# Performance work log

Hardware: AMD Instinct MI355X
Metric: run time of the kernel (lower is better)

The kernel has to match this reference:

```python
import jax, jax.numpy as jnp
import numpy as np

C = 512
IC = C // 2
BN_EPS = 1e-5

def conv1x1(x, w, b):
    # x: (b,c,h,w), w: (o,c), b: (o,)
    return jnp.einsum('bchw,oc->bohw', x, w) + b[None, :, None, None]

def setup_inputs() -> dict:
    key = jax.random.key(0)
    ks = jax.random.split(key, 9)
    b, h, w = 8, 48, 48
    x = jax.random.normal(ks[0], (b, C, h, w), dtype=jnp.float32)
    s = 1.0 / np.sqrt(C)
    g_w = jax.random.normal(ks[1], (IC, C), dtype=jnp.float32) * s
    g_b = jnp.zeros((IC,), jnp.float32)
    theta_w = jax.random.normal(ks[2], (IC, C), dtype=jnp.float32) * s
    theta_b = jnp.zeros((IC,), jnp.float32)
    phi_w = jax.random.normal(ks[3], (IC, C), dtype=jnp.float32) * s
    phi_b = jnp.zeros((IC,), jnp.float32)
    w_w = jax.random.normal(ks[4], (C, IC), dtype=jnp.float32) * (1.0 / np.sqrt(IC))
    w_b = jnp.zeros((C,), jnp.float32)
    # BatchNorm affine params: initialized to 0 per nn.init.constant_ in source
    bn_gamma = jnp.zeros((C,), jnp.float32)
    bn_beta = jnp.zeros((C,), jnp.float32)
    return {"x": x, "g_w": g_w, "g_b": g_b, "theta_w": theta_w, "theta_b": theta_b,
            "phi_w": phi_w, "phi_b": phi_b, "w_w": w_w, "w_b": w_b,
            "bn_gamma": bn_gamma, "bn_beta": bn_beta}

def reference(x, g_w, g_b, theta_w, theta_b, phi_w, phi_b, w_w, w_b, bn_gamma, bn_beta):
    b, c, h, w = x.shape
    hw = h * w
    g_x = conv1x1(x, g_w, g_b).reshape(b, IC, hw).transpose(0, 2, 1)      # (b,hw,ic)
    theta_x = conv1x1(x, theta_w, theta_b).reshape(b, IC, hw).transpose(0, 2, 1)  # (b,hw,ic)
    phi_x = conv1x1(x, phi_w, phi_b).reshape(b, IC, hw)                    # (b,ic,hw)
    f = jnp.einsum('bqc,bck->bqk', theta_x, phi_x)                         # (b,hw,hw), unscaled
    f_div_C = jax.nn.softmax(f, axis=-1)
    y = jnp.einsum('bqk,bkc->bqc', f_div_C, g_x)                           # (b,hw,ic)
    y = y.transpose(0, 2, 1).reshape(b, IC, h, w)
    wy = conv1x1(y, w_w, w_b)                                              # (b,c,h,w)
    # BatchNorm2d in training mode: batch statistics over (b,h,w)
    mean = jnp.mean(wy, axis=(0, 2, 3), keepdims=True)
    var = jnp.var(wy, axis=(0, 2, 3), keepdims=True)
    wy_bn = (wy - mean) / jnp.sqrt(var + BN_EPS)
    wy_bn = wy_bn * bn_gamma[None, :, None, None] + bn_beta[None, :, None, None]
    return wy_bn + x
```

## Files before the change

kernel.cpp:

```cpp
#include <hip/hip_runtime.h>
#include <hip/hip_bf16.h>
#include <stdint.h>

constexpr int Bn  = 8;
constexpr int Cc  = 512;
constexpr int ICc = 256;
constexpr int HWc = 48 * 48;
constexpr float BN_EPS = 1e-5f;

typedef unsigned short u16;
typedef __attribute__((ext_vector_type(8))) short short8;
typedef __attribute__((ext_vector_type(4))) float f32x4;

__device__ __forceinline__ u16 f2bf(float f) {
    uint32_t u = __builtin_bit_cast(uint32_t, f);
    u += 0x7fffu + ((u >> 16) & 1u);
    return (u16)(u >> 16);
}
__device__ __forceinline__ float bf2f(u16 h) {
    uint32_t u = ((uint32_t)h) << 16;
    return __builtin_bit_cast(float, u);
}
__device__ __forceinline__ void load_lds16(const void* g, void* l) {
    __builtin_amdgcn_global_load_lds(
        (const __attribute__((address_space(1))) void*)(uintptr_t)g,
        (__attribute__((address_space(3))) void*)(uintptr_t)l, 16, 0, 0);
}

__global__ __launch_bounds__(256)
void cast_front(const float* __restrict__ th_w, const float* __restrict__ ph_w,
                const float* __restrict__ g_w, const float* __restrict__ th_b,
                const float* __restrict__ ph_b, u16* __restrict__ wcat,
                float* __restrict__ bias_thph) {
    int idx = blockIdx.x * 256 + threadIdx.x;
    if (idx < 98304) {
        const float4* src;
        if (idx < 32768)       src = (const float4*)th_w + idx;
        else if (idx < 65536)  src = (const float4*)ph_w + (idx - 32768);
        else                   src = (const float4*)g_w  + (idx - 65536);
        float4 v = *src;
        ushort4 o;
        o.x = f2bf(v.x); o.y = f2bf(v.y); o.z = f2bf(v.z); o.w = f2bf(v.w);
        ((ushort4*)wcat)[idx] = o;
    } else if (idx < 98816) {
        int i = idx - 98304;
        bias_thph[i] = (i < 256) ? th_b[i] : ph_b[i - 256];
    }
}

__global__ __launch_bounds__(256)
void cast_w(const float* __restrict__ a, u16* __restrict__ out) {
    int idx = blockIdx.x * 256 + threadIdx.x;
    float4 v = ((const float4*)a)[idx];
    ushort4 o;
    o.x = f2bf(v.x); o.y = f2bf(v.y); o.z = f2bf(v.z); o.w = f2bf(v.w);
    ((ushort4*)out)[idx] = o;
}

__global__ __launch_bounds__(256)
void transpose_cast_x(const float* __restrict__ x, u16* __restrict__ xt) {
    __shared__ float t[64][33];
    const int b = blockIdx.z;
    const int p0 = blockIdx.x * 32;
    const int c0 = blockIdx.y * 64;
    const int tx = threadIdx.x & 31, ty = threadIdx.x >> 5;
    const float* xb = x + (size_t)b * Cc * HWc;
#pragma unroll
    for (int r = 0; r < 8; ++r)
        t[r * 8 + ty][tx] = xb[(size_t)(c0 + r * 8 + ty) * HWc + p0 + tx];
    __syncthreads();
    u16* xtb = xt + (size_t)b * HWc * Cc;
    const int cc = (threadIdx.x & 31) * 2, pp = threadIdx.x >> 5;
#pragma unroll
    for (int r = 0; r < 4; ++r) {
        int p = r * 8 + pp;
        ushort2 v;
        v.x = f2bf(t[cc][p]);
        v.y = f2bf(t[cc + 1][p]);
        *(ushort2*)&xtb[(size_t)(p0 + p) * Cc + c0 + cc] = v;
    }
}

template <int TM, int STORE, bool STATS>
__global__ __launch_bounds__(256, 2)
void mfma_gemm(const u16* __restrict__ A, const u16* __restrict__ B,
               void* __restrict__ Cout, const float* __restrict__ bias,
               int bias_mode, int K, int ldA, int ldB, int ldC,
               size_t sA, size_t sB, size_t sC,
               float* __restrict__ s0g, float* __restrict__ s1g) {
    constexpr int MI = TM / 32;
    __shared__ __align__(16) u16 As[TM * 32];
    __shared__ __align__(16) u16 Bs[128 * 32];
    const int bz = blockIdx.z;
    const int m0 = blockIdx.y * TM, n0 = blockIdx.x * 128;
    const u16* Ab = A + (size_t)bz * sA + (size_t)m0 * ldA;
    const u16* Bb = B + (size_t)bz * sB + (size_t)n0 * ldB;
    const int tid = threadIdx.x, lane = tid & 63, w = tid >> 6;
    const int wm = (w & 1) * (TM / 2);
    const int wn = (w >> 1) * 64;
    const int quad = lane >> 4, m16 = lane & 15;

    f32x4 acc[MI][4];
#pragma unroll
    for (int i = 0; i < MI; ++i)
#pragma unroll
        for (int j = 0; j < 4; ++j) acc[i][j] = (f32x4){0.f, 0.f, 0.f, 0.f};

    const int L0 = 2 * w * 64 + lane, L1 = L0 + 64;
    const int br0 = L0 >> 2, bc0 = (L0 & 3) * 8;
    const int br1 = L1 >> 2, bc1 = (L1 & 3) * 8;
    const int ar0 = (TM == 128) ? br0 : (tid >> 2);
    const int ac0 = (TM == 128) ? bc0 : (tid & 3) * 8;

    for (int k0 = 0; k0 < K; k0 += 32) {
        if (TM == 128) {
            load_lds16(Ab + (size_t)ar0 * ldA + k0 + ac0, &As[2 * w * 512]);
            load_lds16(Ab + (size_t)br1 * ldA + k0 + bc1, &As[(2 * w + 1) * 512]);
        } else {
            load_lds16(Ab + (size_t)ar0 * ldA + k0 + ac0, &As[w * 512]);
        }
        load_lds16(Bb + (size_t)br0 * ldB + k0 + bc0, &Bs[2 * w * 512]);
        load_lds16(Bb + (size_t)br1 * ldB + k0 + bc1, &Bs[(2 * w + 1) * 512]);
        __syncthreads();

        short8 af[MI], bfv[4];
#pragma unroll
        for (int i = 0; i < MI; ++i)
            af[i] = *(const short8*)&As[(wm + i * 16 + m16) * 32 + quad * 8];
#pragma unroll
        for (int j = 0; j < 4; ++j)
            bfv[j] = *(const short8*)&Bs[(wn + j * 16 + m16) * 32 + quad * 8];
#pragma unroll
        for (int i = 0; i < MI; ++i)
#pragma unroll
            for (int j = 0; j < 4; ++j)
                acc[i][j] = __builtin_amdgcn_mfma_f32_16x16x32_bf16(
                    af[i], bfv[j], acc[i][j], 0, 0, 0);
        __syncthreads();
    }

    if (bias_mode) {
#pragma unroll
        for (int i = 0; i < MI; ++i)
#pragma unroll
            for (int j = 0; j < 4; ++j)
#pragma unroll
                for (int r = 0; r < 4; ++r)
                    acc[i][j][r] += (bias_mode == 2)
                        ? bias[m0 + wm + i * 16 + quad * 4 + r]
                        : bias[n0 + wn + j * 16 + m16];
    }

    if (STORE == 0) {
        u16* C = (u16*)Cout + (size_t)bz * sC;
#pragma unroll
        for (int i = 0; i < MI; ++i) {
            int m = m0 + wm + i * 16 + quad * 4;
#pragma unroll
            for (int j = 0; j < 4; ++j) {
                int n = n0 + wn + j * 16 + m16;
#pragma unroll
                for (int r = 0; r < 4; ++r)
                    C[(size_t)(m + r) * ldC + n] = f2bf(acc[i][j][r]);
            }
        }
    } else {
        float* C = (float*)Cout + (size_t)bz * sC;
#pragma unroll
        for (int i = 0; i < MI; ++i) {
            int m = m0 + wm + i * 16 + quad * 4;
#pragma unroll
            for (int j = 0; j < 4; ++j) {
                int n = n0 + wn + j * 16 + m16;
#pragma unroll
                for (int r = 0; r < 4; ++r)
                    C[(size_t)(m + r) * ldC + n] = acc[i][j][r];
            }
        }
    }

    if (STATS) {
#pragma unroll
        for (int i = 0; i < MI; ++i) {
#pragma unroll
            for (int r = 0; r < 4; ++r) {
                float v0 = 0.f, v1 = 0.f;
#pragma unroll
                for (int j = 0; j < 4; ++j) {
                    float v = acc[i][j][r];
                    v0 += v;
                    v1 = fmaf(v, v, v1);
                }
#pragma unroll
                for (int off = 8; off; off >>= 1) {
                    v0 += __shfl_down(v0, off, 16);
                    v1 += __shfl_down(v1, off, 16);
                }
                if (m16 == 0) {
                    int m = m0 + wm + i * 16 + quad * 4 + r;
                    atomicAdd(&s0g[m], v0);
                    atomicAdd(&s1g[m], v1);
                }
            }
        }
    }
}

__global__ __launch_bounds__(192)
void softmax_rows(u16* __restrict__ S) {
    const int b = blockIdx.x & 7;
    const int q = blockIdx.x >> 3;
    u16* row = S + ((size_t)b * HWc + q) * (size_t)HWc;
    const int tid = threadIdx.x;

    float v[12];
#pragma unroll
    for (int c = 0; c < 3; ++c) {
        uint2 raw = *(const uint2*)&row[(c * 192 + tid) * 4];
        v[c * 4 + 0] = bf2f((u16)(raw.x & 0xffff));
        v[c * 4 + 1] = bf2f((u16)(raw.x >> 16));
        v[c * 4 + 2] = bf2f((u16)(raw.y & 0xffff));
        v[c * 4 + 3] = bf2f((u16)(raw.y >> 16));
    }
    float m = v[0];
#pragma unroll
    for (int i = 1; i < 12; ++i) m = fmaxf(m, v[i]);
#pragma unroll
    for (int off = 32; off; off >>= 1) m = fmaxf(m, __shfl_down(m, off, 64));
    __shared__ float redm[3], reds[3];
    if ((tid & 63) == 0) redm[tid >> 6] = m;
    __syncthreads();
    m = fmaxf(fmaxf(redm[0], redm[1]), redm[2]);

    float s = 0.f;
#pragma unroll
    for (int i = 0; i < 12; ++i) { v[i] = __expf(v[i] - m); s += v[i]; }
#pragma unroll
    for (int off = 32; off; off >>= 1) s += __shfl_down(s, off, 64);
    if ((tid & 63) == 0) reds[tid >> 6] = s;
    __syncthreads();
    const float rinv = 1.0f / (reds[0] + reds[1] + reds[2]);

#pragma unroll
    for (int c = 0; c < 3; ++c) {
        uint2 o;
        o.x = (uint32_t)f2bf(v[c * 4 + 0] * rinv) |
              ((uint32_t)f2bf(v[c * 4 + 1] * rinv) << 16);
        o.y = (uint32_t)f2bf(v[c * 4 + 2] * rinv) |
              ((uint32_t)f2bf(v[c * 4 + 3] * rinv) << 16);
        *(uint2*)&row[(c * 192 + tid) * 4] = o;
    }
}

__global__ __launch_bounds__(256)
void bn_apply(const float* __restrict__ wy, const float* __restrict__ x,
              const float* __restrict__ s0, const float* __restrict__ s1,
              const float* __restrict__ gamma, const float* __restrict__ beta,
              float* __restrict__ out) {
    const size_t i4 = (size_t)blockIdx.x * 256 + threadIdx.x;
    const size_t base = i4 * 4;
    const int o = (int)((base / HWc) % Cc);
    const float N = (float)(Bn * HWc);
    const float mean = s0[o] / N;
    const float var  = s1[o] / N - mean * mean;
    const float rstd = rsqrtf(var + BN_EPS);
    const float ga = gamma[o];
    const float be = beta[o];
    const float4 w4 = ((const float4*)wy)[i4];
    const float4 x4 = ((const float4*)x)[i4];
    float4 r;
    r.x = (w4.x - mean) * rstd * ga + be + x4.x;
    r.y = (w4.y - mean) * rstd * ga + be + x4.y;
    r.z = (w4.z - mean) * rstd * ga + be + x4.z;
    r.w = (w4.w - mean) * rstd * ga + be + x4.w;
    ((float4*)out)[i4] = r;
}

extern "C" void kernel_launch(void* const* d_in, const int* in_sizes, int n_in,
                              void* d_out, int out_size, void* d_ws, size_t ws_size,
                              hipStream_t stream) {
    const float* x     = (const float*)d_in[0];
    const float* g_w   = (const float*)d_in[1];
    const float* g_b   = (const float*)d_in[2];
    const float* th_w  = (const float*)d_in[3];
    const float* th_b  = (const float*)d_in[4];
    const float* ph_w  = (const float*)d_in[5];
    const float* ph_b  = (const float*)d_in[6];
    const float* w_w   = (const float*)d_in[7];
    const float* w_b   = (const float*)d_in[8];
    const float* gamma = (const float*)d_in[9];
    const float* beta  = (const float*)d_in[10];

    char* base = (char*)d_ws;
    const size_t SZT = (size_t)Bn * HWc * ICc * 2;
    u16* thph = (u16*)base;
    u16* g    = (u16*)(base + 2 * SZT);
    char* Sreg = base + 3 * SZT;
    u16* S    = (u16*)Sreg;
    u16* xt   = (u16*)Sreg;
    u16* wcat = (u16*)(Sreg + (size_t)Bn * HWc * Cc * 2);
    float* bias_thph = (float*)(Sreg + (size_t)Bn * HWc * Cc * 2 + 786432);
    u16* y    = (u16*)base;
    u16* wbf2 = (u16*)(base + SZT);
    float* stats = (float*)(base + SZT + 262144);
    float* wy = (float*)Sreg;

    dim3 blk(256);
    const u16* thphw = wcat;
    const u16* gwb   = wcat + 262144;

    cast_front<<<dim3(386), blk, 0, stream>>>(th_w, ph_w, g_w, th_b, ph_b,
                                              wcat, bias_thph);
    transpose_cast_x<<<dim3(HWc / 32, Cc / 64, Bn), blk, 0, stream>>>(x, xt);

    mfma_gemm<128, 0, false><<<dim3(4, 18, Bn), blk, 0, stream>>>(
        xt, thphw, thph, bias_thph, 1, Cc, Cc, Cc, 512,
        (size_t)HWc * Cc, 0, (size_t)HWc * 512, nullptr, nullptr);

    mfma_gemm<64, 0, false><<<dim3(18, 4, Bn), blk, 0, stream>>>(
        gwb, xt, g, g_b, 2, Cc, Cc, Cc, HWc,
        0, (size_t)HWc * Cc, (size_t)ICc * HWc, nullptr, nullptr);

    mfma_gemm<128, 0, false><<<dim3(18, 18, Bn), blk, 0, stream>>>(
        thph, thph + 256, S, nullptr, 0, ICc, 512, 512, HWc,
        (size_t)HWc * 512, (size_t)HWc * 512, (size_t)HWc * HWc,
        nullptr, nullptr);

    cast_w<<<dim3(128), blk, 0, stream>>>(w_w, wbf2);
    hipMemsetAsync(stats, 0, 2 * Cc * sizeof(float), stream);

    softmax_rows<<<dim3(Bn * HWc), dim3(192), 0, stream>>>(S);

    mfma_gemm<64, 0, false><<<dim3(2, 36, Bn), blk, 0, stream>>>(
        S, g, y, nullptr, 0, HWc, HWc, HWc, ICc,
        (size_t)HWc * HWc, (size_t)ICc * HWc, (size_t)HWc * ICc,
        nullptr, nullptr);

    mfma_gemm<128, 1, true><<<dim3(18, 4, Bn), blk, 0, stream>>>(
        wbf2, y, wy, w_b, 2, ICc, ICc, ICc, HWc,
        0, (size_t)HWc * ICc, (size_t)Cc * HWc, stats, stats + Cc);

    bn_apply<<<dim3((Bn * Cc * HWc) / 4 / 256), blk, 0, stream>>>(
        wy, x, stats, stats + Cc, gamma, beta, (float*)d_out);
}
```

Baseline: 341.1 us.

## Fuse QK^T, softmax and PV into a single flash-attention kernel

Replaces the separate score GEMM, row softmax and PV GEMM with one flash-attention style kernel that keeps scores in registers and LDS and applies an online softmax. This removes writing and re-reading the full bf16 HW×HW score matrix (about 84 MB per batch set) plus two kernel launches. In exchange there are only 288 blocks of 64 queries each, the K/V tiles are loaded without double buffering behind frequent __syncthreads, and the workspace layout is reassigned to non-aliased offsets.

```diff
diff --git a/kernel.cpp b/kernel.cpp
--- a/kernel.cpp
+++ b/kernel.cpp
@@ -16,10 +16,6 @@
     uint32_t u = __builtin_bit_cast(uint32_t, f);
     u += 0x7fffu + ((u >> 16) & 1u);
     return (u16)(u >> 16);
-}
-__device__ __forceinline__ float bf2f(u16 h) {
-    uint32_t u = ((uint32_t)h) << 16;
-    return __builtin_bit_cast(float, u);
 }
 __device__ __forceinline__ void load_lds16(const void* g, void* l) {
     __builtin_amdgcn_global_load_lds(
@@ -206,50 +202,142 @@
     }
 }
 
-__global__ __launch_bounds__(192)
-void softmax_rows(u16* __restrict__ S) {
-    const int b = blockIdx.x & 7;
-    const int q = blockIdx.x >> 3;
-    u16* row = S + ((size_t)b * HWc + q) * (size_t)HWc;
-    const int tid = threadIdx.x;
-
-    float v[12];
-#pragma unroll
-    for (int c = 0; c < 3; ++c) {
-        uint2 raw = *(const uint2*)&row[(c * 192 + tid) * 4];
-        v[c * 4 + 0] = bf2f((u16)(raw.x & 0xffff));
-        v[c * 4 + 1] = bf2f((u16)(raw.x >> 16));
-        v[c * 4 + 2] = bf2f((u16)(raw.y & 0xffff));
-        v[c * 4 + 3] = bf2f((u16)(raw.y >> 16));
-    }
-    float m = v[0];
-#pragma unroll
-    for (int i = 1; i < 12; ++i) m = fmaxf(m, v[i]);
-#pragma unroll
-    for (int off = 32; off; off >>= 1) m = fmaxf(m, __shfl_down(m, off, 64));
-    __shared__ float redm[3], reds[3];
-    if ((tid & 63) == 0) redm[tid >> 6] = m;
+__global__ __launch_bounds__(256, 2)
+void flash_attn(const u16* __restrict__ thph, const u16* __restrict__ g,
+                u16* __restrict__ y) {
+    __shared__ __align__(16) u16 smem[25088];
+    const int bz = blockIdx.y;
+    const int q0 = blockIdx.x * 64;
+    const u16* Qb = thph + (size_t)bz * HWc * 512 + (size_t)q0 * 512;
+    const u16* Kb = thph + (size_t)bz * HWc * 512 + 256;
+    const u16* Vb = g + (size_t)bz * ICc * HWc;
+    const int tid = threadIdx.x, lane = tid & 63, w = tid >> 6;
+    const int quad = lane >> 4, m16 = lane & 15;
+    const int wm = w * 16;
+
+#pragma unroll
+    for (int t = 0; t < 8; ++t) {
+        int L = (w * 8 + t) * 64 + lane;
+        int row = L >> 5, col = (L & 31) * 8;
+        load_lds16(Qb + (size_t)row * 512 + col, &smem[8192 + (w * 8 + t) * 512]);
+    }
     __syncthreads();
-    m = fmaxf(fmaxf(redm[0], redm[1]), redm[2]);
-
-    float s = 0.f;
-#pragma unroll
-    for (int i = 0; i < 12; ++i) { v[i] = __expf(v[i] - m); s += v[i]; }
-#pragma unroll
-    for (int off = 32; off; off >>= 1) s += __shfl_down(s, off, 64);
-    if ((tid & 63) == 0) reds[tid >> 6] = s;
+    short8 qf[8];
+#pragma unroll
+    for (int c = 0; c < 8; ++c)
+        qf[c] = *(const short8*)&smem[8192 + (wm + m16) * 256 + c * 32 + quad * 8];
     __syncthreads();
-    const float rinv = 1.0f / (reds[0] + reds[1] + reds[2]);
-
-#pragma unroll
-    for (int c = 0; c < 3; ++c) {
-        uint2 o;
-        o.x = (uint32_t)f2bf(v[c * 4 + 0] * rinv) |
-              ((uint32_t)f2bf(v[c * 4 + 1] * rinv) << 16);
-        o.y = (uint32_t)f2bf(v[c * 4 + 2] * rinv) |
-              ((uint32_t)f2bf(v[c * 4 + 3] * rinv) << 16);
-        *(uint2*)&row[(c * 192 + tid) * 4] = o;
-    }
+
+    f32x4 O[16];
+#pragma unroll
+    for (int i = 0; i < 16; ++i) O[i] = (f32x4){0.f, 0.f, 0.f, 0.f};
+    float mrow[4] = {-1e30f, -1e30f, -1e30f, -1e30f};
+    float lrow[4] = {0.f, 0.f, 0.f, 0.f};
+
+    for (int kt = 0; kt < 18; ++kt) {
+        const u16* Kt = Kb + (size_t)kt * 128 * 512;
+        f32x4 Sa[8];
+#pragma unroll
+        for (int j = 0; j < 8; ++j) Sa[j] = (f32x4){0.f, 0.f, 0.f, 0.f};
+
+#pragma unroll
+        for (int kc = 0; kc < 4; ++kc) {
+#pragma unroll
+            for (int h = 0; h < 2; ++h) {
+                int cdim = (kc * 2 + h) * 32;
+#pragma unroll
+                for (int t = 0; t < 2; ++t) {
+                    int L = (w * 2 + t) * 64 + lane;
+                    int row = L >> 2, col = (L & 3) * 8;
+                    load_lds16(Kt + (size_t)row * 512 + cdim + col,
+                               &smem[h * 4096 + (w * 2 + t) * 512]);
+                }
+            }
+            __syncthreads();
+#pragma unroll
+            for (int h = 0; h < 2; ++h)
+#pragma unroll
+                for (int j = 0; j < 8; ++j) {
+                    short8 kf = *(const short8*)
+                        &smem[h * 4096 + (j * 16 + m16) * 32 + quad * 8];
+                    Sa[j] = __builtin_amdgcn_mfma_f32_16x16x32_bf16(
+                        qf[kc * 2 + h], kf, Sa[j], 0, 0, 0);
+                }
+            __syncthreads();
+        }
+
+        float alpha[4];
+#pragma unroll
+        for (int r = 0; r < 4; ++r) {
+            float tm = Sa[0][r];
+#pragma unroll
+            for (int j = 1; j < 8; ++j) tm = fmaxf(tm, Sa[j][r]);
+#pragma unroll
+            for (int off = 1; off < 16; off <<= 1)
+                tm = fmaxf(tm, __shfl_xor(tm, off, 16));
+            float nm = fmaxf(mrow[r], tm);
+            alpha[r] = __expf(mrow[r] - nm);
+            mrow[r] = nm;
+            float ps = 0.f;
+#pragma unroll
+            for (int j = 0; j < 8; ++j) {
+                float p = __expf(Sa[j][r] - nm);
+                Sa[j][r] = p;
+                ps += p;
+            }
+#pragma unroll
+            for (int off = 1; off < 16; off <<= 1)
+                ps += __shfl_xor(ps, off, 16);
+            lrow[r] = lrow[r] * alpha[r] + ps;
+        }
+#pragma unroll
+        for (int j2 = 0; j2 < 16; ++j2)
+#pragma unroll
+            for (int r = 0; r < 4; ++r) O[j2][r] *= alpha[r];
+
+        u16* Pw = &smem[16384 + w * 2176];
+#pragma unroll
+        for (int j = 0; j < 8; ++j)
+#pragma unroll
+            for (int r = 0; r < 4; ++r)
+                Pw[(quad * 4 + r) * 136 + j * 16 + m16] = f2bf(Sa[j][r]);
+        short8 pf[4];
+#pragma unroll
+        for (int c2 = 0; c2 < 4; ++c2)
+            pf[c2] = *(const short8*)&Pw[m16 * 136 + c2 * 32 + quad * 8];
+
+#pragma unroll
+        for (int c2 = 0; c2 < 4; ++c2) {
+            int keyc = kt * 128 + c2 * 32;
+#pragma unroll
+            for (int t = 0; t < 4; ++t) {
+                int L = (w * 4 + t) * 64 + lane;
+                int row = L >> 2, col = (L & 3) * 8;
+                load_lds16(Vb + (size_t)row * HWc + keyc + col,
+                           &smem[8192 + (w * 4 + t) * 512]);
+            }
+            __syncthreads();
+#pragma unroll
+            for (int j2 = 0; j2 < 16; ++j2) {
+                short8 vf = *(const short8*)
+                    &smem[8192 + (j2 * 16 + m16) * 32 + quad * 8];
+                O[j2] = __builtin_amdgcn_mfma_f32_16x16x32_bf16(
+                    pf[c2], vf, O[j2], 0, 0, 0);
+            }
+            __syncthreads();
+        }
+    }
+
+    float rinv[4];
+#pragma unroll
+    for (int r = 0; r < 4; ++r) rinv[r] = 1.0f / lrow[r];
+    u16* yb = y + ((size_t)bz * HWc + q0 + wm) * ICc;
+#pragma unroll
+    for (int j2 = 0; j2 < 16; ++j2)
+#pragma unroll
+        for (int r = 0; r < 4; ++r)
+            yb[(size_t)(quad * 4 + r) * ICc + j2 * 16 + m16] =
+                f2bf(O[j2][r] * rinv[r]);
 }
 
 __global__ __launch_bounds__(256)
@@ -292,18 +380,15 @@
     const float* beta  = (const float*)d_in[10];
 
     char* base = (char*)d_ws;
-    const size_t SZT = (size_t)Bn * HWc * ICc * 2;
     u16* thph = (u16*)base;
-    u16* g    = (u16*)(base + 2 * SZT);
-    char* Sreg = base + 3 * SZT;
-    u16* S    = (u16*)Sreg;
-    u16* xt   = (u16*)Sreg;
-    u16* wcat = (u16*)(Sreg + (size_t)Bn * HWc * Cc * 2);
-    float* bias_thph = (float*)(Sreg + (size_t)Bn * HWc * Cc * 2 + 786432);
-    u16* y    = (u16*)base;
-    u16* wbf2 = (u16*)(base + SZT);
-    float* stats = (float*)(base + SZT + 262144);
-    float* wy = (float*)Sreg;
+    u16* g    = (u16*)(base + 18874368);
+    u16* xt   = (u16*)(base + 28311552);
+    u16* wcat = (u16*)(base + 47185920);
+    float* bias_thph = (float*)(base + 47972352);
+    u16* wbf2 = (u16*)(base + 47974400);
+    float* stats = (float*)(base + 48236544);
+    u16* y    = (u16*)(base + 48240640);
+    float* wy = (float*)(base + 57677824);
 
     dim3 blk(256);
     const u16* thphw = wcat;
@@ -311,6 +396,8 @@
 
     cast_front<<<dim3(386), blk, 0, stream>>>(th_w, ph_w, g_w, th_b, ph_b,
                                               wcat, bias_thph);
+    cast_w<<<dim3(128), blk, 0, stream>>>(w_w, wbf2);
+    hipMemsetAsync(stats, 0, 2 * Cc * sizeof(float), stream);
     transpose_cast_x<<<dim3(HWc / 32, Cc / 64, Bn), blk, 0, stream>>>(x, xt);
 
     mfma_gemm<128, 0, false><<<dim3(4, 18, Bn), blk, 0, stream>>>(
@@ -321,20 +408,7 @@
         gwb, xt, g, g_b, 2, Cc, Cc, Cc, HWc,
         0, (size_t)HWc * Cc, (size_t)ICc * HWc, nullptr, nullptr);
 
-    mfma_gemm<128, 0, false><<<dim3(18, 18, Bn), blk, 0, stream>>>(
-        thph, thph + 256, S, nullptr, 0, ICc, 512, 512, HWc,
-        (size_t)HWc * 512, (size_t)HWc * 512, (size_t)HWc * HWc,
-        nullptr, nullptr);
-
-    cast_w<<<dim3(128), blk, 0, stream>>>(w_w, wbf2);
-    hipMemsetAsync(stats, 0, 2 * Cc * sizeof(float), stream);
-
-    softmax_rows<<<dim3(Bn * HWc), dim3(192), 0, stream>>>(S);
-
-    mfma_gemm<64, 0, false><<<dim3(2, 36, Bn), blk, 0, stream>>>(
-        S, g, y, nullptr, 0, HWc, HWc, HWc, ICc,
-        (size_t)HWc * HWc, (size_t)ICc * HWc, (size_t)HWc * ICc,
-        nullptr, nullptr);
+    flash_attn<<<dim3(HWc / 64, Bn), blk, 0, stream>>>(thph, g, y);
 
     mfma_gemm<128, 1, true><<<dim3(18, 4, Bn), blk, 0, stream>>>(
         wbf2, y, wy, w_b, 2, ICc, ICc, ICc, HWc,
```

Result: slower. 361.1 us (+5.9%).

## Fuse row softmax into PV GEMM with online-softmax rescaling

Applied to the files above, without the earlier changes.

Removes the standalone softmax kernel, which read and wrote the full bf16 score matrix, and computes the softmax on the fly inside a new PV GEMM using a running max and sum per row with accumulator rescaling. This saves one full read-write pass over the large S tensor. In exchange it adds exp and shuffle work to every k-tile of the GEMM and uses a 2x2 warp tiling on a 64x128 tile with no double buffering. Each row's exps are also recomputed in both N-blocks (ICc/128 = 2).

```diff
diff --git a/kernel.cpp b/kernel.cpp
--- a/kernel.cpp
+++ b/kernel.cpp
@@ -206,49 +206,98 @@
     }
 }
 
-__global__ __launch_bounds__(192)
-void softmax_rows(u16* __restrict__ S) {
-    const int b = blockIdx.x & 7;
-    const int q = blockIdx.x >> 3;
-    u16* row = S + ((size_t)b * HWc + q) * (size_t)HWc;
-    const int tid = threadIdx.x;
-
-    float v[12];
-#pragma unroll
-    for (int c = 0; c < 3; ++c) {
-        uint2 raw = *(const uint2*)&row[(c * 192 + tid) * 4];
-        v[c * 4 + 0] = bf2f((u16)(raw.x & 0xffff));
-        v[c * 4 + 1] = bf2f((u16)(raw.x >> 16));
-        v[c * 4 + 2] = bf2f((u16)(raw.y & 0xffff));
-        v[c * 4 + 3] = bf2f((u16)(raw.y >> 16));
-    }
-    float m = v[0];
-#pragma unroll
-    for (int i = 1; i < 12; ++i) m = fmaxf(m, v[i]);
-#pragma unroll
-    for (int off = 32; off; off >>= 1) m = fmaxf(m, __shfl_down(m, off, 64));
-    __shared__ float redm[3], reds[3];
-    if ((tid & 63) == 0) redm[tid >> 6] = m;
-    __syncthreads();
-    m = fmaxf(fmaxf(redm[0], redm[1]), redm[2]);
-
-    float s = 0.f;
-#pragma unroll
-    for (int i = 0; i < 12; ++i) { v[i] = __expf(v[i] - m); s += v[i]; }
-#pragma unroll
-    for (int off = 32; off; off >>= 1) s += __shfl_down(s, off, 64);
-    if ((tid & 63) == 0) reds[tid >> 6] = s;
-    __syncthreads();
-    const float rinv = 1.0f / (reds[0] + reds[1] + reds[2]);
-
-#pragma unroll
-    for (int c = 0; c < 3; ++c) {
-        uint2 o;
-        o.x = (uint32_t)f2bf(v[c * 4 + 0] * rinv) |
-              ((uint32_t)f2bf(v[c * 4 + 1] * rinv) << 16);
-        o.y = (uint32_t)f2bf(v[c * 4 + 2] * rinv) |
-              ((uint32_t)f2bf(v[c * 4 + 3] * rinv) << 16);
-        *(uint2*)&row[(c * 192 + tid) * 4] = o;
+__global__ __launch_bounds__(256, 2)
+void pv_gemm(const u16* __restrict__ S, const u16* __restrict__ g,
+             u16* __restrict__ y) {
+    __shared__ __align__(16) u16 As[64 * 32];
+    __shared__ __align__(16) u16 Bs[128 * 32];
+    const int bz = blockIdx.z;
+    const int m0 = blockIdx.y * 64, n0 = blockIdx.x * 128;
+    const u16* Ab = S + (size_t)bz * HWc * HWc + (size_t)m0 * HWc;
+    const u16* Bb = g + (size_t)bz * ICc * HWc + (size_t)n0 * HWc;
+    const int tid = threadIdx.x, lane = tid & 63, w = tid >> 6;
+    const int wm = (w & 1) * 32;
+    const int wn = (w >> 1) * 64;
+    const int quad = lane >> 4, m16 = lane & 15;
+
+    f32x4 acc[2][4];
+#pragma unroll
+    for (int i = 0; i < 2; ++i)
+#pragma unroll
+        for (int j = 0; j < 4; ++j) acc[i][j] = (f32x4){0.f, 0.f, 0.f, 0.f};
+    float mrow[2] = {-1e30f, -1e30f};
+    float lrow[2] = {0.f, 0.f};
+
+    const int ar0 = tid >> 2, ac0 = (tid & 3) * 8;
+    const int L0 = 2 * w * 64 + lane, L1 = L0 + 64;
+    const int br0 = L0 >> 2, bc0 = (L0 & 3) * 8;
+    const int br1 = L1 >> 2, bc1 = (L1 & 3) * 8;
+
+    for (int k0 = 0; k0 < HWc; k0 += 32) {
+        load_lds16(Ab + (size_t)ar0 * HWc + k0 + ac0, &As[w * 512]);
+        load_lds16(Bb + (size_t)br0 * HWc + k0 + bc0, &Bs[2 * w * 512]);
+        load_lds16(Bb + (size_t)br1 * HWc + k0 + bc1, &Bs[(2 * w + 1) * 512]);
+        __syncthreads();
+
+        short8 pf[2];
+#pragma unroll
+        for (int i = 0; i < 2; ++i) {
+            short8 a8 = *(const short8*)&As[(wm + i * 16 + m16) * 32 + quad * 8];
+            float av[8];
+#pragma unroll
+            for (int j = 0; j < 8; ++j) av[j] = bf2f((u16)a8[j]);
+            float tm = av[0];
+#pragma unroll
+            for (int j = 1; j < 8; ++j) tm = fmaxf(tm, av[j]);
+            tm = fmaxf(tm, __shfl_xor(tm, 16, 64));
+            tm = fmaxf(tm, __shfl_xor(tm, 32, 64));
+            float nm = fmaxf(mrow[i], tm);
+            float alpha = __expf(mrow[i] - nm);
+            mrow[i] = nm;
+            float ps = 0.f;
+#pragma unroll
+            for (int j = 0; j < 8; ++j) {
+                float p = __expf(av[j] - nm);
+                pf[i][j] = (short)f2bf(p);
+                ps += p;
+            }
+            ps += __shfl_xor(ps, 16, 64);
+            ps += __shfl_xor(ps, 32, 64);
+            lrow[i] = lrow[i] * alpha + ps;
+#pragma unroll
+            for (int r = 0; r < 4; ++r) {
+                float ar = __shfl(alpha, quad * 4 + r, 16);
+#pragma unroll
+                for (int j = 0; j < 4; ++j) acc[i][j][r] *= ar;
+            }
+        }
+
+        short8 bfv[4];
+#pragma unroll
+        for (int j = 0; j < 4; ++j)
+            bfv[j] = *(const short8*)&Bs[(wn + j * 16 + m16) * 32 + quad * 8];
+#pragma unroll
+        for (int i = 0; i < 2; ++i)
+#pragma unroll
+            for (int j = 0; j < 4; ++j)
+                acc[i][j] = __builtin_amdgcn_mfma_f32_16x16x32_bf16(
+                    pf[i], bfv[j], acc[i][j], 0, 0, 0);
+        __syncthreads();
+    }
+
+#pragma unroll
+    for (int i = 0; i < 2; ++i) {
+        float rl = 1.0f / lrow[i];
+#pragma unroll
+        for (int r = 0; r < 4; ++r) {
+            float rr = __shfl(rl, quad * 4 + r, 16);
+            int m = m0 + wm + i * 16 + quad * 4 + r;
+#pragma unroll
+            for (int j = 0; j < 4; ++j) {
+                int n = n0 + wn + j * 16 + m16;
+                y[((size_t)bz * HWc + m) * ICc + n] = f2bf(acc[i][j][r] * rr);
+            }
+        }
     }
 }
 
@@ -329,12 +378,7 @@
     cast_w<<<dim3(128), blk, 0, stream>>>(w_w, wbf2);
     hipMemsetAsync(stats, 0, 2 * Cc * sizeof(float), stream);
 
-    softmax_rows<<<dim3(Bn * HWc), dim3(192), 0, stream>>>(S);
-
-    mfma_gemm<64, 0, false><<<dim3(2, 36, Bn), blk, 0, stream>>>(
-        S, g, y, nullptr, 0, HWc, HWc, HWc, ICc,
-        (size_t)HWc * HWc, (size_t)ICc * HWc, (size_t)HWc * ICc,
-        nullptr, nullptr);
+    pv_gemm<<<dim3(ICc / 128, HWc / 64, Bn), blk, 0, stream>>>(S, g, y);
 
     mfma_gemm<128, 1, true><<<dim3(18, 4, Bn), blk, 0, stream>>>(
         wbf2, y, wy, w_b, 2, ICc, ICc, ICc, HWc,
```

Result: slower. 387.8 us (+13.7%).
